# Performance work log

Hardware: AMD Instinct MI355X
Metric: run time of the kernel (lower is better)

## Reference

```python
import jax, jax.numpy as jnp
from jax import lax
import numpy as np

K = 3          # kernel_size
PAD = 1        # K // 2
MAX_OFFSET = 0.1
EPS = 1e-8


def setup_inputs() -> dict:
    key = jax.random.key(0)
    k0, k1, k2 = jax.random.split(key, 3)
    B, C, H, W = 4, 64, 256, 256
    Cmid = C // 4
    x = jax.random.normal(k0, (B, C, H, W), jnp.float32)
    # offset_predictor: Conv2d(C+9, C//4, 3, pad=1) -> LeakyReLU(0.2) -> Conv2d(C//4, 2, 3, pad=1) -> Tanh
    w1 = jax.random.normal(k1, (Cmid, C + K * K, 3, 3), jnp.float32) * 0.05
    b1 = jnp.zeros((Cmid,), jnp.float32)
    w2 = jax.random.normal(k2, (2, Cmid, 3, 3), jnp.float32) * 0.05
    b2 = jnp.zeros((2,), jnp.float32)
    return {"x": x, "w1": w1, "b1": b1, "w2": w2, "b2": b2}


def _conv2d(x, w, b):
    # NCHW, OIHW, stride 1, pad 1 (SAME for 3x3)
    out = lax.conv_general_dilated(x, w, (1, 1), ((PAD, PAD), (PAD, PAD)),
                                   dimension_numbers=("NCHW", "OIHW", "NCHW"))
    return out + b[None, :, None, None]


def _local_cosine_similarity(x):
    # F.unfold with zero padding: neighbors[k] at spatial shift (di-1, dj-1), row-major k = di*K + dj
    B, C, H, W = x.shape
    xp = jnp.pad(x, ((0, 0), (0, 0), (PAD, PAD), (PAD, PAD)))
    neighbors = jnp.stack([xp[:, :, di:di + H, dj:dj + W]
                           for di in range(K) for dj in range(K)], axis=2)  # (B,C,9,H,W)
    center = x[:, :, None, :, :]                                            # (B,C,1,H,W)
    numerator = jnp.sum(neighbors * center, axis=1)                         # (B,9,H,W)
    center_norm = jnp.sqrt(jnp.sum(x * x, axis=1)) + EPS                    # (B,H,W)
    neighbor_norm = jnp.sqrt(jnp.sum(neighbors * neighbors, axis=1)) + EPS  # (B,9,H,W)
    return numerator / (center_norm[:, None] * neighbor_norm)               # (B,9,H,W)


def _grid_sample_border(x, grid):
    # bilinear, padding_mode='border', align_corners=True; grid: (B,H,W,2) with (gx,gy) in [-1,1]
    B, C, H, W = x.shape
    ix = (grid[..., 0] + 1.0) * 0.5 * (W - 1)
    iy = (grid[..., 1] + 1.0) * 0.5 * (H - 1)
    ix = jnp.clip(ix, 0.0, W - 1)
    iy = jnp.clip(iy, 0.0, H - 1)
    x0f = jnp.floor(ix); y0f = jnp.floor(iy)
    wx = ix - x0f; wy = iy - y0f
    x0 = x0f.astype(jnp.int32); y0 = y0f.astype(jnp.int32)
    x1 = jnp.minimum(x0 + 1, W - 1); y1 = jnp.minimum(y0 + 1, H - 1)

    def gather(img, yy, xx):  # img (C,H,W), yy/xx (H,W) -> (C,H,W)
        return img[:, yy, xx]

    g = jax.vmap(gather)
    v00 = g(x, y0, x0); v01 = g(x, y0, x1)
    v10 = g(x, y1, x0); v11 = g(x, y1, x1)
    wx = wx[:, None]; wy = wy[:, None]  # broadcast over channel dim
    return ((1 - wy) * ((1 - wx) * v00 + wx * v01)
            + wy * ((1 - wx) * v10 + wx * v11))


def reference(x, w1, b1, w2, b2):
    B, C, H, W = x.shape
    sim = _local_cosine_similarity(x)                       # (B,9,H,W)
    features = jnp.concatenate([x, sim], axis=1)            # (B,C+9,H,W)
    h = _conv2d(features, w1, b1)
    h = jnp.where(h >= 0, h, 0.2 * h)                       # LeakyReLU(0.2)
    offset = jnp.tanh(_conv2d(h, w2, b2)) * MAX_OFFSET      # (B,2,H,W)
    gy, gx = jnp.meshgrid(jnp.linspace(-1.0, 1.0, H),
                          jnp.linspace(-1.0, 1.0, W), indexing="ij")
    base_grid = jnp.stack([gx, gy], axis=-1)[None]          # (1,H,W,2)
    offset_grid = base_grid + jnp.transpose(offset, (0, 2, 3, 1))
    return _grid_sample_border(x, offset_grid)
```

## Files before the change

### kernel.cpp

```cpp
#include <hip/hip_runtime.h>
#include <math.h>

#define B 4
#define C 64
#define H 256
#define W 256
#define CMID 16
#define CIN 73
#define HW (H*W)
#define NW (CIN*9*CMID)
#define XS_STRIDE 260
#define XSR 258
#define XSW 256

__global__ void transpose_w1_kernel(const float* __restrict__ w1, float* __restrict__ wt) {
    int tid = blockIdx.x * blockDim.x + threadIdx.x;
    if (tid >= NW) return;
    int co = tid & (CMID - 1);
    int rest = tid >> 4;
    int ci = rest / 9;
    int k = rest - ci * 9;
    wt[tid] = w1[(co * CIN + ci) * 9 + k];
}

__device__ __forceinline__ void read_patch9(const float* __restrict__ base, float v[9]) {
#pragma unroll
    for (int r = 0; r < 3; ++r) {
        v[r * 3 + 0] = base[r * XSR + 0];
        v[r * 3 + 1] = base[r * XSR + 1];
        v[r * 3 + 2] = base[r * XSR + 2];
    }
}

__global__ __launch_bounds__(256) void sim_kernel(const float* __restrict__ x,
                                                  float* __restrict__ sim) {
    __shared__ float xs[2][4][3 * XSR];

    int bid = blockIdx.x;
    int sb = (bid & 7) * 128 + (bid >> 3);
    int b = sb >> 8;
    int y = sb & 255;
    int tid = threadIdx.x;

    const float* xb = x + (size_t)b * C * HW;

    bool rv[3];
    long off[3];
#pragma unroll
    for (int j = 0; j < 3; ++j) {
        int grow = y - 1 + j;
        rv[j] = (grow >= 0) && (grow < H);
        off[j] = (long)grow * W + tid;
    }

    if (tid < 48) {
        int e = tid & 1;
        int r = (tid >> 1) % 3;
        int q = (tid >> 1) / 3;
        (&xs[0][0][0])[q * (3 * XSR) + r * XSR + (e ? 257 : 0)] = 0.f;
    }

    float dot[9], nsq[9];
    float csq = 0.f;
#pragma unroll
    for (int i = 0; i < 9; ++i) { dot[i] = nsq[i] = 0.f; }

    float p[12];
#pragma unroll
    for (int k = 0; k < 4; ++k)
#pragma unroll
        for (int j = 0; j < 3; ++j)
            p[k * 3 + j] = rv[j] ? xb[(size_t)k * HW + off[j]] : 0.f;

    int cur = 0;
#pragma unroll 1
    for (int cc = 0; cc < C; cc += 4) {
#pragma unroll
        for (int k = 0; k < 4; ++k)
#pragma unroll
            for (int j = 0; j < 3; ++j)
                xs[cur][k][j * XSR + 1 + tid] = p[k * 3 + j];
        __syncthreads();

        if (cc + 4 < C) {
#pragma unroll
            for (int k = 0; k < 4; ++k)
#pragma unroll
                for (int j = 0; j < 3; ++j)
                    p[k * 3 + j] = rv[j] ? xb[(size_t)(cc + 4 + k) * HW + off[j]] : 0.f;
        }

#pragma unroll
        for (int k = 0; k < 4; ++k) {
            float v[9];
            read_patch9(&xs[cur][k][tid], v);
            float cv = v[4];
            csq = fmaf(cv, cv, csq);
#pragma unroll
            for (int kk = 0; kk < 9; ++kk) {
                if (kk == 4) continue;
                dot[kk] = fmaf(cv, v[kk], dot[kk]);
                nsq[kk] = fmaf(v[kk], v[kk], nsq[kk]);
            }
        }
        cur ^= 1;
    }

    dot[4] = csq;
    nsq[4] = csq;
    float cn = sqrtf(csq) + 1e-8f;
    float* so = sim + (size_t)b * 9 * HW + (size_t)y * W + tid;
#pragma unroll
    for (int kk = 0; kk < 9; ++kk)
        so[(size_t)kk * HW] = dot[kk] / (cn * (sqrtf(nsq[kk]) + 1e-8f));
}

__device__ __forceinline__ float dpp_shr1(float x) {
    return __int_as_float(__builtin_amdgcn_update_dpp(
        0, __float_as_int(x), 0x138, 0xf, 0xf, false));
}
__device__ __forceinline__ float dpp_shl1(float x) {
    return __int_as_float(__builtin_amdgcn_update_dpp(
        0, __float_as_int(x), 0x130, 0xf, 0xf, false));
}

__device__ __forceinline__ void conv1_co4(const float* __restrict__ chbase, int l,
                                          const float4 wv[9], float4 acc[2][4]) {
    float v[4][6];
#pragma unroll
    for (int r = 0; r < 4; ++r) {
        const float* rp = chbase + r * XSW;
        float4 m = *(const float4*)(rp + 4 * l);
        v[r][1] = m.x; v[r][2] = m.y; v[r][3] = m.z; v[r][4] = m.w;
        v[r][0] = dpp_shr1(m.w);
        v[r][5] = dpp_shl1(m.x);
    }
#pragma unroll
    for (int kr = 0; kr < 3; ++kr)
#pragma unroll
        for (int kc = 0; kc < 3; ++kc) {
            float4 w = wv[kr * 3 + kc];
#pragma unroll
            for (int rr = 0; rr < 2; ++rr)
#pragma unroll
                for (int cc = 0; cc < 4; ++cc) {
                    float a = v[rr + kr][cc + kc];
                    acc[rr][cc].x = fmaf(a, w.x, acc[rr][cc].x);
                    acc[rr][cc].y = fmaf(a, w.y, acc[rr][cc].y);
                    acc[rr][cc].z = fmaf(a, w.z, acc[rr][cc].z);
                    acc[rr][cc].w = fmaf(a, w.w, acc[rr][cc].w);
                }
        }
}

__global__ __launch_bounds__(256) void conv1_kernel(const float* __restrict__ x,
                                                    const float* __restrict__ sim,
                                                    const float* __restrict__ wt,
                                                    const float* __restrict__ b1,
                                                    float* __restrict__ h) {
    __shared__ __align__(16) float xs[2][2][4 * XSW];

    int tid = threadIdx.x;
    int l = tid & 63;
    int wid = tid >> 6;
    int bid = blockIdx.x;
    int sb = (bid & 7) * 64 + (bid >> 3);
    int b  = sb >> 7;
    int y0 = (sb & 127) << 1;

    int vz;
    asm volatile("v_mov_b32 %0, 0" : "=v"(vz));
    const float4* wq = (const float4*)wt + vz;

    const float* gx = x + (size_t)b * C * HW;
    const float* gs = sim + (size_t)b * 9 * HW;

    int grow = y0 - 1 + wid;
    bool rvw = (grow >= 0) && (grow < H);
    size_t goff = (size_t)grow * W + 4 * l;

    float4 bias = ((const float4*)b1)[wid];
    float4 acc[2][4];
#pragma unroll
    for (int rr = 0; rr < 2; ++rr)
#pragma unroll
        for (int cc = 0; cc < 4; ++cc) acc[rr][cc] = bias;

    float4 wA[9], wB[9];
#pragma unroll
    for (int k = 0; k < 9; ++k) wA[k] = wq[k * 4 + wid];

    float4 p0 = make_float4(0.f, 0.f, 0.f, 0.f), p1 = p0;
    if (rvw) {
        p0 = *(const float4*)(gx + goff);
        p1 = *(const float4*)(gx + HW + goff);
    }

    int cur = 0;
#pragma unroll 1
    for (int cc2 = 0; cc2 < 72; cc2 += 2) {
        *(float4*)&xs[cur][0][wid * XSW + 4 * l] = p0;
        *(float4*)&xs[cur][1][wid * XSW + 4 * l] = p1;
        __syncthreads();

        {
            int ci = cc2 + 2;
            p0 = make_float4(0.f, 0.f, 0.f, 0.f);
            if (rvw)
                p0 = (ci < C) ? *(const float4*)(gx + (size_t)ci * HW + goff)
                              : *(const float4*)(gs + (size_t)(ci - C) * HW + goff);
            int cj = cc2 + 3;
            p1 = make_float4(0.f, 0.f, 0.f, 0.f);
            if (rvw && cj < CIN)
                p1 = (cj < C) ? *(const float4*)(gx + (size_t)cj * HW + goff)
                              : *(const float4*)(gs + (size_t)(cj - C) * HW + goff);
        }

#pragma unroll
        for (int k = 0; k < 9; ++k) wB[k] = wq[((cc2 + 1) * 9 + k) * 4 + wid];

        conv1_co4(&xs[cur][0][0], l, wA, acc);

#pragma unroll
        for (int k = 0; k < 9; ++k) wA[k] = wq[((cc2 + 2) * 9 + k) * 4 + wid];

        conv1_co4(&xs[cur][1][0], l, wB, acc);

        cur ^= 1;
    }

    *(float4*)&xs[cur][0][wid * XSW + 4 * l] = p0;
    __syncthreads();
    conv1_co4(&xs[cur][0][0], l, wA, acc);

    float* ho = h + ((size_t)b * CMID + 4 * wid) * HW + (size_t)y0 * W + 4 * l;
#pragma unroll
    for (int rr = 0; rr < 2; ++rr)
#pragma unroll
        for (int j = 0; j < 4; ++j) {
            float4 o;
            o.x = ((const float*)&acc[rr][0])[j];
            o.y = ((const float*)&acc[rr][1])[j];
            o.z = ((const float*)&acc[rr][2])[j];
            o.w = ((const float*)&acc[rr][3])[j];
            o.x = o.x >= 0.f ? o.x : 0.2f * o.x;
            o.y = o.y >= 0.f ? o.y : 0.2f * o.y;
            o.z = o.z >= 0.f ? o.z : 0.2f * o.z;
            o.w = o.w >= 0.f ? o.w : 0.2f * o.w;
            *(float4*)(ho + (size_t)j * HW + (size_t)rr * W) = o;
        }
}

__device__ __forceinline__ void read_patch_lds(const float* __restrict__ xsbuf,
                                               int rl, int px, float v[3][4]) {
    const float* pb = xsbuf + rl * XS_STRIDE + px;
#pragma unroll
    for (int r = 0; r < 3; ++r) {
        float2 p0 = *(const float2*)(pb + r * XS_STRIDE);
        float2 p1 = *(const float2*)(pb + r * XS_STRIDE + 2);
        v[r][0] = p0.x; v[r][1] = p0.y; v[r][2] = p1.x; v[r][3] = p1.y;
    }
}

__global__ __launch_bounds__(256) void offset_kernel(const float* __restrict__ h,
                                                     const float* __restrict__ w2,
                                                     const float* __restrict__ b2,
                                                     float2* __restrict__ off_buf) {
    __shared__ float lw2[CMID * 9 * 2];
    __shared__ float xs[2][4 * XS_STRIDE];

    int tid = threadIdx.x;
    for (int i = tid; i < CMID * 9 * 2; i += 256) {
        int co = i & 1;
        int rest = i >> 1;
        int ci = rest / 9;
        int kk = rest - ci * 9;
        lw2[i] = w2[(co * CMID + ci) * 9 + kk];
    }

    int bid = blockIdx.x;
    int sb = (bid & 7) * 64 + (bid >> 3);
    int b  = sb >> 7;
    int y0 = (sb & 127) << 1;
    int srow = tid >> 6;
    int sx4  = (tid & 63) << 2;
    int rl = tid >> 7;
    int px = (tid & 127) << 1;
    int y  = y0 + rl;

    int grow = y0 - 1 + srow;
    bool gvalid = (grow >= 0) && (grow < H);
    const float* gh = h + (size_t)b * CMID * HW + (size_t)grow * W + sx4;

    if (tid < 16) {
        int bu = tid >> 3, r = (tid >> 1) & 3, e = (tid & 1) ? 257 : 0;
        xs[bu][r * XS_STRIDE + e] = 0.f;
    }

    float s0x = b2[0], s0y = b2[1], s1x = b2[0], s1y = b2[1];

    float4 r4 = make_float4(0.f, 0.f, 0.f, 0.f);
    if (gvalid) r4 = *(const float4*)gh;

    int cur = 0;
#pragma unroll 1
    for (int ci = 0; ci < CMID; ++ci) {
        float* dst = &xs[cur][srow * XS_STRIDE + 1 + sx4];
        dst[0] = r4.x; dst[1] = r4.y; dst[2] = r4.z; dst[3] = r4.w;
        __syncthreads();
        if (ci + 1 < CMID) {
            r4 = make_float4(0.f, 0.f, 0.f, 0.f);
            if (gvalid) r4 = *(const float4*)(gh + (size_t)(ci + 1) * HW);
        }
        float v[3][4];
        read_patch_lds(xs[cur], rl, px, v);
#pragma unroll
        for (int kr = 0; kr < 3; ++kr)
#pragma unroll
            for (int kc = 0; kc < 3; ++kc) {
                float2 wv = *(const float2*)(lw2 + (ci * 9 + kr * 3 + kc) * 2);
                s0x = fmaf(v[kr][kc],     wv.x, s0x);
                s0y = fmaf(v[kr][kc],     wv.y, s0y);
                s1x = fmaf(v[kr][kc + 1], wv.x, s1x);
                s1y = fmaf(v[kr][kc + 1], wv.y, s1y);
            }
        cur ^= 1;
    }

    float ix0 = (float)px       + 0.1f * tanhf(s0x) * (0.5f * (float)(W - 1));
    float iy0 = (float)y        + 0.1f * tanhf(s0y) * (0.5f * (float)(H - 1));
    float ix1 = (float)(px + 1) + 0.1f * tanhf(s1x) * (0.5f * (float)(W - 1));
    float iy1 = (float)y        + 0.1f * tanhf(s1y) * (0.5f * (float)(H - 1));
    ix0 = fminf(fmaxf(ix0, 0.f), (float)(W - 1));
    iy0 = fminf(fmaxf(iy0, 0.f), (float)(H - 1));
    ix1 = fminf(fmaxf(ix1, 0.f), (float)(W - 1));
    iy1 = fminf(fmaxf(iy1, 0.f), (float)(H - 1));

    float4* op = (float4*)(off_buf + (size_t)b * HW + (size_t)y * W + px);
    *op = make_float4(ix0, iy0, ix1, iy1);
}

#define SROWS 35
__global__ __launch_bounds__(256) void sample_kernel(const float* __restrict__ x,
                                                     const float2* __restrict__ off_buf,
                                                     float* __restrict__ out) {
    __shared__ float xs[SROWS * 256];

    int bid = blockIdx.x;
    int sb = (bid & 7) * 16 + (bid >> 3);
    int b  = sb >> 5;
    int ty = sb & 31;
    int cg = blockIdx.y;
    int tid = threadIdx.x;

    int ybase = ty << 3;
    int lo = ybase - 13;

    int a00[8], a01[8], a10[8], a11[8];
    float wx[8], wy[8];
    const float2* ob2 = off_buf + (size_t)b * HW + (size_t)ybase * W + tid;
#pragma unroll
    for (int r = 0; r < 8; ++r) {
        float2 o = ob2[r * W];
        float xf = floorf(o.x), yf = floorf(o.y);
        wx[r] = o.x - xf; wy[r] = o.y - yf;
        int x0 = (int)xf, yy0 = (int)yf;
        int x1 = min(x0 + 1, W - 1), yy1 = min(yy0 + 1, H - 1);
        int r0 = (yy0 - lo) << 8, r1 = (yy1 - lo) << 8;
        a00[r] = r0 + x0; a01[r] = r0 + x1;
        a10[r] = r1 + x0; a11[r] = r1 + x1;
    }

    const float* xb = x + ((size_t)b * C + cg * 4) * HW;
    float* outb = out + ((size_t)b * C + cg * 4) * HW + (size_t)ybase * W + tid;

#pragma unroll 1
    for (int c = 0; c < 4; ++c) {
        __syncthreads();
        const float* src = xb + (size_t)c * HW;
        for (int j = tid; j < SROWS * 64; j += 256) {
            int row = j >> 6, x4 = (j & 63) << 2;
            int grw = min(max(lo + row, 0), H - 1);
            *(float4*)&xs[(row << 8) + x4] = *(const float4*)(src + (size_t)grw * W + x4);
        }
        __syncthreads();
        float* oc = outb + (size_t)c * HW;
#pragma unroll
        for (int r = 0; r < 8; ++r) {
            float v00 = xs[a00[r]], v01 = xs[a01[r]];
            float v10 = xs[a10[r]], v11 = xs[a11[r]];
            float top = fmaf(wx[r], v01 - v00, v00);
            float bot = fmaf(wx[r], v11 - v10, v10);
            oc[r * W] = fmaf(wy[r], bot - top, top);
        }
    }
}

extern "C" void kernel_launch(void* const* d_in, const int* in_sizes, int n_in,
                              void* d_out, int out_size, void* d_ws, size_t ws_size,
                              hipStream_t stream) {
    const float* x  = (const float*)d_in[0];
    const float* w1 = (const float*)d_in[1];
    const float* b1 = (const float*)d_in[2];
    const float* w2 = (const float*)d_in[3];
    const float* b2 = (const float*)d_in[4];
    float* out = (float*)d_out;

    float* ws  = (float*)d_ws;
    float* wt  = ws;
    float* sim = ws + 16384;
    float* h   = sim + (size_t)B * 9 * HW;
    float2* off_buf = (float2*)(h + (size_t)B * CMID * HW);

    transpose_w1_kernel<<<(NW + 255) / 256, 256, 0, stream>>>(w1, wt);

    sim_kernel<<<B * H, 256, 0, stream>>>(x, sim);
    conv1_kernel<<<512, 256, 0, stream>>>(x, sim, wt, b1, h);
    offset_kernel<<<512, 256, 0, stream>>>(h, w2, b2, off_buf);
    sample_kernel<<<dim3(128, 16), 256, 0, stream>>>(x, off_buf, out);
}
```

Baseline: 241.7 us.

## Load conv1 input rows directly into registers, dropping LDS staging and barriers

```diff
diff --git a/kernel.cpp b/kernel.cpp
--- a/kernel.cpp
+++ b/kernel.cpp
@@ -11,7 +11,6 @@
 #define NW (CIN*9*CMID)
 #define XS_STRIDE 260
 #define XSR 258
-#define XSW 256
 
 __global__ void transpose_w1_kernel(const float* __restrict__ w1, float* __restrict__ wt) {
     int tid = blockIdx.x * blockDim.x + threadIdx.x;
@@ -124,17 +123,17 @@
         0, __float_as_int(x), 0x130, 0xf, 0xf, false));
 }
 
-__device__ __forceinline__ void conv1_co4(const float* __restrict__ chbase, int l,
-                                          const float4 wv[9], float4 acc[2][4]) {
-    float v[4][6];
+__device__ __forceinline__ void extract6(const float4 m[4], float v[4][6]) {
 #pragma unroll
     for (int r = 0; r < 4; ++r) {
-        const float* rp = chbase + r * XSW;
-        float4 m = *(const float4*)(rp + 4 * l);
-        v[r][1] = m.x; v[r][2] = m.y; v[r][3] = m.z; v[r][4] = m.w;
-        v[r][0] = dpp_shr1(m.w);
-        v[r][5] = dpp_shl1(m.x);
-    }
+        v[r][1] = m[r].x; v[r][2] = m[r].y; v[r][3] = m[r].z; v[r][4] = m[r].w;
+        v[r][0] = dpp_shr1(m[r].w);
+        v[r][5] = dpp_shl1(m[r].x);
+    }
+}
+
+__device__ __forceinline__ void conv1_fma(const float v[4][6], const float4 wv[9],
+                                          float4 acc[2][4]) {
 #pragma unroll
     for (int kr = 0; kr < 3; ++kr)
 #pragma unroll
@@ -153,13 +152,11 @@
         }
 }
 
-__global__ __launch_bounds__(256) void conv1_kernel(const float* __restrict__ x,
-                                                    const float* __restrict__ sim,
-                                                    const float* __restrict__ wt,
-                                                    const float* __restrict__ b1,
-                                                    float* __restrict__ h) {
-    __shared__ __align__(16) float xs[2][2][4 * XSW];
-
+__global__ __launch_bounds__(256, 2) void conv1_kernel(const float* __restrict__ x,
+                                                       const float* __restrict__ sim,
+                                                       const float* __restrict__ wt,
+                                                       const float* __restrict__ b1,
+                                                       float* __restrict__ h) {
     int tid = threadIdx.x;
     int l = tid & 63;
     int wid = tid >> 6;
@@ -175,9 +172,14 @@
     const float* gx = x + (size_t)b * C * HW;
     const float* gs = sim + (size_t)b * 9 * HW;
 
-    int grow = y0 - 1 + wid;
-    bool rvw = (grow >= 0) && (grow < H);
-    size_t goff = (size_t)grow * W + 4 * l;
+    bool rv[4];
+    size_t off[4];
+#pragma unroll
+    for (int j = 0; j < 4; ++j) {
+        int grow = y0 - 1 + j;
+        rv[j] = (grow >= 0) && (grow < H);
+        off[j] = (size_t)grow * W + 4 * l;
+    }
 
     float4 bias = ((const float4*)b1)[wid];
     float4 acc[2][4];
@@ -190,48 +192,49 @@
 #pragma unroll
     for (int k = 0; k < 9; ++k) wA[k] = wq[k * 4 + wid];
 
-    float4 p0 = make_float4(0.f, 0.f, 0.f, 0.f), p1 = p0;
-    if (rvw) {
-        p0 = *(const float4*)(gx + goff);
-        p1 = *(const float4*)(gx + HW + goff);
-    }
-
-    int cur = 0;
+    const float4 z4 = make_float4(0.f, 0.f, 0.f, 0.f);
+    float4 pA[4], pB[4];
+#pragma unroll
+    for (int j = 0; j < 4; ++j) pA[j] = rv[j] ? *(const float4*)(gx + off[j]) : z4;
+#pragma unroll
+    for (int j = 0; j < 4; ++j) pB[j] = rv[j] ? *(const float4*)(gx + HW + off[j]) : z4;
+
 #pragma unroll 1
     for (int cc2 = 0; cc2 < 72; cc2 += 2) {
-        *(float4*)&xs[cur][0][wid * XSW + 4 * l] = p0;
-        *(float4*)&xs[cur][1][wid * XSW + 4 * l] = p1;
-        __syncthreads();
-
+        float vA[4][6];
+        extract6(pA, vA);
         {
             int ci = cc2 + 2;
-            p0 = make_float4(0.f, 0.f, 0.f, 0.f);
-            if (rvw)
-                p0 = (ci < C) ? *(const float4*)(gx + (size_t)ci * HW + goff)
-                              : *(const float4*)(gs + (size_t)(ci - C) * HW + goff);
+            const float* cb = (ci < C) ? (gx + (size_t)ci * HW)
+                                       : (gs + (size_t)(ci - C) * HW);
+#pragma unroll
+            for (int j = 0; j < 4; ++j) pA[j] = rv[j] ? *(const float4*)(cb + off[j]) : z4;
+        }
+#pragma unroll
+        for (int k = 0; k < 9; ++k) wB[k] = wq[((cc2 + 1) * 9 + k) * 4 + wid];
+        conv1_fma(vA, wA, acc);
+
+        float vB[4][6];
+        extract6(pB, vB);
+        {
             int cj = cc2 + 3;
-            p1 = make_float4(0.f, 0.f, 0.f, 0.f);
-            if (rvw && cj < CIN)
-                p1 = (cj < C) ? *(const float4*)(gx + (size_t)cj * HW + goff)
-                              : *(const float4*)(gs + (size_t)(cj - C) * HW + goff);
-        }
-
-#pragma unroll
-        for (int k = 0; k < 9; ++k) wB[k] = wq[((cc2 + 1) * 9 + k) * 4 + wid];
-
-        conv1_co4(&xs[cur][0][0], l, wA, acc);
-
+            if (cj < CIN) {
+                const float* cb = (cj < C) ? (gx + (size_t)cj * HW)
+                                           : (gs + (size_t)(cj - C) * HW);
+#pragma unroll
+                for (int j = 0; j < 4; ++j) pB[j] = rv[j] ? *(const float4*)(cb + off[j]) : z4;
+            }
+        }
 #pragma unroll
         for (int k = 0; k < 9; ++k) wA[k] = wq[((cc2 + 2) * 9 + k) * 4 + wid];
-
-        conv1_co4(&xs[cur][1][0], l, wB, acc);
-
-        cur ^= 1;
-    }
-
-    *(float4*)&xs[cur][0][wid * XSW + 4 * l] = p0;
-    __syncthreads();
-    conv1_co4(&xs[cur][0][0], l, wA, acc);
+        conv1_fma(vB, wB, acc);
+    }
+
+    {
+        float vA[4][6];
+        extract6(pA, vA);
+        conv1_fma(vA, wA, acc);
+    }
 
     float* ho = h + ((size_t)b * CMID + 4 * wid) * HW + (size_t)y0 * W + 4 * l;
 #pragma unroll
```

New measurement: 256.7 us. 6.2% more time.
